# Optimization experiments

Hardware: AMD Instinct MI355X
Metric: run time of the kernel (lower is better)

## Reference

```python
import jax, jax.numpy as jnp
import numpy as np

PRECISION = 127.0  # number of discrete pulse-width levels per unit weight


def pwb_quantize(w):
    """PWBMapper: constrain weight to [-1, 1] and snap to `precision` levels."""
    return jnp.round(jnp.clip(w, -1.0, 1.0) * PRECISION) / PRECISION


def setup_inputs() -> dict:
    key = jax.random.key(0)
    kx, kw, kb = jax.random.split(key, 3)
    B, D_in, D_out = 32768, 1024, 128
    x = jax.random.normal(kx, (B, D_in), dtype=jnp.float32)
    # random_normal_initializer default stddev is small; scale a bit but keep in clip range
    W = jax.random.normal(kw, (D_in, D_out), dtype=jnp.float32) * 0.05
    b = jax.random.normal(kb, (D_out,), dtype=jnp.float32) * 0.05
    return {"x": x, "W": W, "b": b}


def reference(x, W, b):
    # Each neuron n.step(data) = dot(quantized weight column, data);
    # bias_neuron.step(e_i) = quantized bias[i].  Activation is identity (None).
    Wq = pwb_quantize(W)          # [D_in, D_out]
    bq = pwb_quantize(b)          # [D_out]
    return x @ Wq + bq            # [B, D_out]
```

## Files before the change

### kernel.cpp

```cpp
#include <hip/hip_runtime.h>
#include <cstdint>

#define K_DIM 1024
#define N_DIM 128
#define BM 64
#define BK 32
#define NT (K_DIM / BK)

typedef __attribute__((ext_vector_type(8))) short bf16x8;
typedef __attribute__((ext_vector_type(4))) float f32x4;
typedef unsigned short u16;
typedef unsigned int u32;

__device__ __forceinline__ float pwbq(float w) {
  w = fminf(fmaxf(w, -1.0f), 1.0f);
  return rintf(w * 127.0f) * (1.0f / 127.0f);
}

__device__ __forceinline__ u16 f2bf(float f) {
  union { float f; u32 u; } v; v.f = f;
  u32 r = v.u + 0x7FFFu + ((v.u >> 16) & 1u);
  return (u16)(r >> 16);
}

__global__ __launch_bounds__(256) void quantW_kernel(const float* __restrict__ W,
                                                     u16* __restrict__ Wimg) {
  int H = blockIdx.x * 256 + threadIdx.x;
  int t = H >> 12;
  int h = H & 4095;
  int col = h >> 5;
  int j = (h & 31) ^ ((col & 3) << 3);
  int k = t * BK + j;
  Wimg[H] = f2bf(pwbq(W[k * N_DIM + col]));
}

__global__ __launch_bounds__(256) void naive_kernel(const float* __restrict__ x,
                                                    const float* __restrict__ W,
                                                    const float* __restrict__ b,
                                                    float* __restrict__ out, int total) {
  int idx = blockIdx.x * 256 + threadIdx.x;
  if (idx >= total) return;
  int m = idx >> 7, n = idx & 127;
  float acc = pwbq(b[n]);
  for (int k = 0; k < K_DIM; ++k)
    acc = fmaf(x[(size_t)m * K_DIM + k], pwbq(W[k * N_DIM + n]), acc);
  out[idx] = acc;
}

__global__ __launch_bounds__(256, 2) void pwb_gemm(
    const float* __restrict__ x,
    const u16* __restrict__ Wimg,
    const float* __restrict__ bias,
    float* __restrict__ out) {

  __shared__ __align__(16) float As[4][BM * BK];
  __shared__ __align__(16) u16   Bs[4][N_DIM * BK];

  const int tid  = threadIdx.x;
  const int lane = tid & 63;
  const int wid  = tid >> 6;
  const int wm   = wid >> 1;
  const int wn   = wid & 1;
  const int m0   = blockIdx.x * BM;
  const int l15  = lane & 15;
  const int lg   = lane >> 4;

  auto stage = [&](int s, int t) {
#pragma unroll
    for (int i = 0; i < 2; ++i) {
      int cd  = i * 256 + tid;
      int row = cd >> 3;
      int cs  = (cd & 7) ^ (row & 7);
      const float* srcA = x + (size_t)(m0 + row) * K_DIM + t * BK + cs * 4;
      __builtin_amdgcn_global_load_lds(
          (const __attribute__((address_space(1))) void*)srcA,
          (__attribute__((address_space(3))) void*)(&As[s][cd * 4]), 16, 0, 0);
    }
#pragma unroll
    for (int i = 0; i < 2; ++i) {
      int cd = i * 256 + tid;
      const u16* srcB = Wimg + (size_t)t * (N_DIM * BK) + cd * 8;
      __builtin_amdgcn_global_load_lds(
          (const __attribute__((address_space(1))) void*)srcB,
          (__attribute__((address_space(3))) void*)(&Bs[s][cd * 8]), 16, 0, 0);
    }
  };

  f32x4 acc[2][4] = {};

  stage(0, 0);
  stage(1, 1);

#pragma unroll 2
  for (int t = 0; t < NT; ++t) {
    const int buf = t & 3;
    if (t + 2 < NT) {
      stage((t + 2) & 3, t + 2);
      asm volatile("s_waitcnt vmcnt(8)" ::: "memory");
    } else if (t + 1 < NT) {
      asm volatile("s_waitcnt vmcnt(4)" ::: "memory");
    } else {
      asm volatile("s_waitcnt vmcnt(0)" ::: "memory");
    }
    asm volatile("s_barrier" ::: "memory");

    bf16x8 a[2];
#pragma unroll
    for (int q = 0; q < 2; ++q) {
      int row  = wm * 32 + q * 16 + l15;
      int base = row * 128 + lg * 32;
      int sw   = (row & 7) << 4;
      f32x4 f0 = *(const f32x4*)((const char*)&As[buf][0] + (base ^ sw));
      f32x4 f1 = *(const f32x4*)((const char*)&As[buf][0] + ((base + 16) ^ sw));
      union { bf16x8 v; u16 h[8]; } pa;
#pragma unroll
      for (int j = 0; j < 4; ++j) {
        pa.h[j]     = f2bf(f0[j]);
        pa.h[4 + j] = f2bf(f1[j]);
      }
      a[q] = pa.v;
    }

    bf16x8 bfr[4];
#pragma unroll
    for (int f = 0; f < 4; ++f) {
      int col  = wn * 64 + f * 16 + l15;
      int hoff = col * 32 + ((lg * 8) ^ ((col & 3) << 3));
      bfr[f] = *(const bf16x8*)(&Bs[buf][hoff]);
    }

#pragma unroll
    for (int q = 0; q < 2; ++q)
#pragma unroll
      for (int f = 0; f < 4; ++f)
        acc[q][f] = __builtin_amdgcn_mfma_f32_16x16x32_bf16(a[q], bfr[f], acc[q][f], 0, 0, 0);
  }

  float bq[4];
#pragma unroll
  for (int f = 0; f < 4; ++f) bq[f] = pwbq(bias[wn * 64 + f * 16 + l15]);

#pragma unroll
  for (int q = 0; q < 2; ++q) {
    int gr0 = m0 + wm * 32 + q * 16 + lg * 4;
#pragma unroll
    for (int f = 0; f < 4; ++f) {
      int gc = wn * 64 + f * 16 + l15;
#pragma unroll
      for (int j = 0; j < 4; ++j) {
        out[(size_t)(gr0 + j) * N_DIM + gc] = acc[q][f][j] + bq[f];
      }
    }
  }
}

extern "C" void kernel_launch(void* const* d_in, const int* in_sizes, int n_in,
                              void* d_out, int out_size, void* d_ws, size_t ws_size,
                              hipStream_t stream) {
  const float* x = (const float*)d_in[0];
  const float* W = (const float*)d_in[1];
  const float* b = (const float*)d_in[2];
  float* out = (float*)d_out;

  const int M = in_sizes[0] / K_DIM;
  const int grid = M / BM;

  const size_t need = (size_t)K_DIM * N_DIM * sizeof(u16);
  if (d_ws != nullptr && ws_size >= need) {
    u16* Wimg = (u16*)d_ws;
    quantW_kernel<<<(K_DIM * N_DIM) / 256, 256, 0, stream>>>(W, Wimg);
    pwb_gemm<<<grid, 256, 0, stream>>>(x, Wimg, b, out);
  } else {
    int total = M * N_DIM;
    naive_kernel<<<(total + 255) / 256, 256, 0, stream>>>(x, W, b, out, total);
  }
}
```

Measured before the change: 35.70 us.

## Replace LDS-staged GEMM with direct global-to-register loads and smaller tiles

Removes shared memory staging and barriers: each wave loads its A rows and B fragments directly from global memory into registers with a three-slot register prefetch ring. The M tile shrinks to 32 rows so there are more blocks, with each of the four waves owning 32 output columns, and occupancy is raised to four blocks per CU. Conversion to bf16 now uses the packed HIP intrinsic. The trade-off is that the x rows are loaded redundantly by all four waves (four times the global/L2 traffic for A), with no barrier-based reuse through LDS.

```diff
diff --git a/kernel.cpp b/kernel.cpp
--- a/kernel.cpp
+++ b/kernel.cpp
@@ -1,11 +1,11 @@
 #include <hip/hip_runtime.h>
+#include <hip/hip_bf16.h>
 #include <cstdint>
 
 #define K_DIM 1024
 #define N_DIM 128
-#define BM 64
-#define BK 32
-#define NT (K_DIM / BK)
+#define BM 32
+#define NT 32
 
 typedef __attribute__((ext_vector_type(8))) short bf16x8;
 typedef __attribute__((ext_vector_type(4))) float f32x4;
@@ -27,11 +27,9 @@
                                                      u16* __restrict__ Wimg) {
   int H = blockIdx.x * 256 + threadIdx.x;
   int t = H >> 12;
-  int h = H & 4095;
-  int col = h >> 5;
-  int j = (h & 31) ^ ((col & 3) << 3);
-  int k = t * BK + j;
-  Wimg[H] = f2bf(pwbq(W[k * N_DIM + col]));
+  int col = (H >> 5) & 127;
+  int j = H & 31;
+  Wimg[H] = f2bf(pwbq(W[(t * 32 + j) * N_DIM + col]));
 }
 
 __global__ __launch_bounds__(256) void naive_kernel(const float* __restrict__ x,
@@ -47,105 +45,79 @@
   out[idx] = acc;
 }
 
-__global__ __launch_bounds__(256, 2) void pwb_gemm(
+__global__ __launch_bounds__(256, 4) void pwb_gemm(
     const float* __restrict__ x,
     const u16* __restrict__ Wimg,
     const float* __restrict__ bias,
     float* __restrict__ out) {
 
-  __shared__ __align__(16) float As[4][BM * BK];
-  __shared__ __align__(16) u16   Bs[4][N_DIM * BK];
-
   const int tid  = threadIdx.x;
   const int lane = tid & 63;
   const int wid  = tid >> 6;
-  const int wm   = wid >> 1;
-  const int wn   = wid & 1;
   const int m0   = blockIdx.x * BM;
   const int l15  = lane & 15;
   const int lg   = lane >> 4;
 
-  auto stage = [&](int s, int t) {
+  const float* pa0 = x + (size_t)(m0 + l15) * K_DIM + lg * 8;
+  const float* pa1 = pa0 + (size_t)16 * K_DIM;
+  const u16*   pb0 = Wimg + (wid * 32 + l15) * 32 + lg * 8;
+  const u16*   pb1 = pb0 + 16 * 32;
+
+  f32x4  af[3][2][2];
+  bf16x8 bf[3][2];
+  f32x4  acc[2][2] = {};
+
+#define LOADT(S, T)                                                        \
+  do {                                                                     \
+    const float* a0 = pa0 + (T) * 32;                                      \
+    const float* a1 = pa1 + (T) * 32;                                      \
+    af[S][0][0] = *(const f32x4*)(a0);                                     \
+    af[S][0][1] = *(const f32x4*)(a0 + 4);                                 \
+    af[S][1][0] = *(const f32x4*)(a1);                                     \
+    af[S][1][1] = *(const f32x4*)(a1 + 4);                                 \
+    bf[S][0] = *(const bf16x8*)(pb0 + (T) * 4096);                         \
+    bf[S][1] = *(const bf16x8*)(pb1 + (T) * 4096);                         \
+  } while (0)
+
+  LOADT(0, 0);
+  LOADT(1, 1);
+
 #pragma unroll
-    for (int i = 0; i < 2; ++i) {
-      int cd  = i * 256 + tid;
-      int row = cd >> 3;
-      int cs  = (cd & 7) ^ (row & 7);
-      const float* srcA = x + (size_t)(m0 + row) * K_DIM + t * BK + cs * 4;
-      __builtin_amdgcn_global_load_lds(
-          (const __attribute__((address_space(1))) void*)srcA,
-          (__attribute__((address_space(3))) void*)(&As[s][cd * 4]), 16, 0, 0);
-    }
-#pragma unroll
-    for (int i = 0; i < 2; ++i) {
-      int cd = i * 256 + tid;
-      const u16* srcB = Wimg + (size_t)t * (N_DIM * BK) + cd * 8;
-      __builtin_amdgcn_global_load_lds(
-          (const __attribute__((address_space(1))) void*)srcB,
-          (__attribute__((address_space(3))) void*)(&Bs[s][cd * 8]), 16, 0, 0);
-    }
-  };
-
-  f32x4 acc[2][4] = {};
-
-  stage(0, 0);
-  stage(1, 1);
-
-#pragma unroll 2
   for (int t = 0; t < NT; ++t) {
-    const int buf = t & 3;
-    if (t + 2 < NT) {
-      stage((t + 2) & 3, t + 2);
-      asm volatile("s_waitcnt vmcnt(8)" ::: "memory");
-    } else if (t + 1 < NT) {
-      asm volatile("s_waitcnt vmcnt(4)" ::: "memory");
-    } else {
-      asm volatile("s_waitcnt vmcnt(0)" ::: "memory");
-    }
-    asm volatile("s_barrier" ::: "memory");
+    const int s = t % 3;
+    if (t + 2 < NT) LOADT((t + 2) % 3, t + 2);
 
     bf16x8 a[2];
 #pragma unroll
     for (int q = 0; q < 2; ++q) {
-      int row  = wm * 32 + q * 16 + l15;
-      int base = row * 128 + lg * 32;
-      int sw   = (row & 7) << 4;
-      f32x4 f0 = *(const f32x4*)((const char*)&As[buf][0] + (base ^ sw));
-      f32x4 f1 = *(const f32x4*)((const char*)&As[buf][0] + ((base + 16) ^ sw));
-      union { bf16x8 v; u16 h[8]; } pa;
-#pragma unroll
-      for (int j = 0; j < 4; ++j) {
-        pa.h[j]     = f2bf(f0[j]);
-        pa.h[4 + j] = f2bf(f1[j]);
-      }
+      union { bf16x8 v; __hip_bfloat162 p[4]; } pa;
+      f32x4 f0 = af[s][q][0];
+      f32x4 f1 = af[s][q][1];
+      pa.p[0] = __float22bfloat162_rn(make_float2(f0[0], f0[1]));
+      pa.p[1] = __float22bfloat162_rn(make_float2(f0[2], f0[3]));
+      pa.p[2] = __float22bfloat162_rn(make_float2(f1[0], f1[1]));
+      pa.p[3] = __float22bfloat162_rn(make_float2(f1[2], f1[3]));
       a[q] = pa.v;
-    }
-
-    bf16x8 bfr[4];
-#pragma unroll
-    for (int f = 0; f < 4; ++f) {
-      int col  = wn * 64 + f * 16 + l15;
-      int hoff = col * 32 + ((lg * 8) ^ ((col & 3) << 3));
-      bfr[f] = *(const bf16x8*)(&Bs[buf][hoff]);
     }
 
 #pragma unroll
     for (int q = 0; q < 2; ++q)
 #pragma unroll
-      for (int f = 0; f < 4; ++f)
-        acc[q][f] = __builtin_amdgcn_mfma_f32_16x16x32_bf16(a[q], bfr[f], acc[q][f], 0, 0, 0);
+      for (int f = 0; f < 2; ++f)
+        acc[q][f] = __builtin_amdgcn_mfma_f32_16x16x32_bf16(a[q], bf[s][f], acc[q][f], 0, 0, 0);
   }
+#undef LOADT
 
-  float bq[4];
+  float bq[2];
 #pragma unroll
-  for (int f = 0; f < 4; ++f) bq[f] = pwbq(bias[wn * 64 + f * 16 + l15]);
+  for (int f = 0; f < 2; ++f) bq[f] = pwbq(bias[wid * 32 + f * 16 + l15]);
 
 #pragma unroll
   for (int q = 0; q < 2; ++q) {
-    int gr0 = m0 + wm * 32 + q * 16 + lg * 4;
+    int gr0 = m0 + q * 16 + lg * 4;
 #pragma unroll
-    for (int f = 0; f < 4; ++f) {
-      int gc = wn * 64 + f * 16 + l15;
+    for (int f = 0; f < 2; ++f) {
+      int gc = wid * 32 + f * 16 + l15;
 #pragma unroll
       for (int j = 0; j < 4; ++j) {
         out[(size_t)(gr0 + j) * N_DIM + gc] = acc[q][f][j] + bq[f];
```

Result: slower. 82.04 us (+129.8%).

## Halve M tile, use triple-buffered LDS with single barrier, packed bf16 conversion

Applied to the files above, without the earlier changes.

Reduces the block row tile from 64 to 32 rows, so each wave handles one 16-row A fragment, and raises the launch bound to 4 blocks per SIMD group. The LDS ring shrinks from four to three stages. The next-next stage is now issued after the barrier, which lets a single barrier per iteration protect buffer reuse. The manual fp32-to-bf16 rounding is replaced by packed __float22bfloat162_rn conversions, and the K loop is fully unrolled. The goal is more occupancy and more blocks to hide memory latency, at the cost of reloading the full W tile for every 32 rows, which doubles B traffic per output row.

```diff
diff --git a/kernel.cpp b/kernel.cpp
--- a/kernel.cpp
+++ b/kernel.cpp
@@ -1,9 +1,10 @@
 #include <hip/hip_runtime.h>
+#include <hip/hip_bf16.h>
 #include <cstdint>
 
 #define K_DIM 1024
 #define N_DIM 128
-#define BM 64
+#define BM 32
 #define BK 32
 #define NT (K_DIM / BK)
 
@@ -47,14 +48,14 @@
   out[idx] = acc;
 }
 
-__global__ __launch_bounds__(256, 2) void pwb_gemm(
+__global__ __launch_bounds__(256, 4) void pwb_gemm(
     const float* __restrict__ x,
     const u16* __restrict__ Wimg,
     const float* __restrict__ bias,
     float* __restrict__ out) {
 
-  __shared__ __align__(16) float As[4][BM * BK];
-  __shared__ __align__(16) u16   Bs[4][N_DIM * BK];
+  __shared__ __align__(16) float As[3][BM * BK];
+  __shared__ __align__(16) u16   Bs[3][N_DIM * BK];
 
   const int tid  = threadIdx.x;
   const int lane = tid & 63;
@@ -66,9 +67,8 @@
   const int lg   = lane >> 4;
 
   auto stage = [&](int s, int t) {
-#pragma unroll
-    for (int i = 0; i < 2; ++i) {
-      int cd  = i * 256 + tid;
+    {
+      int cd  = tid;
       int row = cd >> 3;
       int cs  = (cd & 7) ^ (row & 7);
       const float* srcA = x + (size_t)(m0 + row) * K_DIM + t * BK + cs * 4;
@@ -86,71 +86,50 @@
     }
   };
 
-  f32x4 acc[2][4] = {};
+  f32x4 acc[4] = {};
 
   stage(0, 0);
   stage(1, 1);
 
-#pragma unroll 2
+#pragma unroll
   for (int t = 0; t < NT; ++t) {
-    const int buf = t & 3;
-    if (t + 2 < NT) {
-      stage((t + 2) & 3, t + 2);
-      asm volatile("s_waitcnt vmcnt(8)" ::: "memory");
-    } else if (t + 1 < NT) {
-      asm volatile("s_waitcnt vmcnt(4)" ::: "memory");
-    } else {
-      asm volatile("s_waitcnt vmcnt(0)" ::: "memory");
-    }
+    const int buf = t % 3;
+
+    if (t + 1 < NT) asm volatile("s_waitcnt vmcnt(3)" ::: "memory");
+    else            asm volatile("s_waitcnt vmcnt(0)" ::: "memory");
     asm volatile("s_barrier" ::: "memory");
 
-    bf16x8 a[2];
-#pragma unroll
-    for (int q = 0; q < 2; ++q) {
-      int row  = wm * 32 + q * 16 + l15;
-      int base = row * 128 + lg * 32;
-      int sw   = (row & 7) << 4;
-      f32x4 f0 = *(const f32x4*)((const char*)&As[buf][0] + (base ^ sw));
-      f32x4 f1 = *(const f32x4*)((const char*)&As[buf][0] + ((base + 16) ^ sw));
-      union { bf16x8 v; u16 h[8]; } pa;
-#pragma unroll
-      for (int j = 0; j < 4; ++j) {
-        pa.h[j]     = f2bf(f0[j]);
-        pa.h[4 + j] = f2bf(f1[j]);
-      }
-      a[q] = pa.v;
-    }
+    if (t + 2 < NT) stage((t + 2) % 3, t + 2);
 
-    bf16x8 bfr[4];
+    const int row  = wm * 16 + l15;
+    const int base = row * 128 + lg * 32;
+    const int sw   = (row & 7) << 4;
+    f32x4 f0 = *(const f32x4*)((const char*)&As[buf][0] + (base ^ sw));
+    f32x4 f1 = *(const f32x4*)((const char*)&As[buf][0] + ((base + 16) ^ sw));
+    union { bf16x8 v; __hip_bfloat162 p[4]; } pa;
+    pa.p[0] = __float22bfloat162_rn(make_float2(f0[0], f0[1]));
+    pa.p[1] = __float22bfloat162_rn(make_float2(f0[2], f0[3]));
+    pa.p[2] = __float22bfloat162_rn(make_float2(f1[0], f1[1]));
+    pa.p[3] = __float22bfloat162_rn(make_float2(f1[2], f1[3]));
+    bf16x8 a = pa.v;
+
 #pragma unroll
     for (int f = 0; f < 4; ++f) {
       int col  = wn * 64 + f * 16 + l15;
       int hoff = col * 32 + ((lg * 8) ^ ((col & 3) << 3));
-      bfr[f] = *(const bf16x8*)(&Bs[buf][hoff]);
+      bf16x8 bfr = *(const bf16x8*)(&Bs[buf][hoff]);
+      acc[f] = __builtin_amdgcn_mfma_f32_16x16x32_bf16(a, bfr, acc[f], 0, 0, 0);
     }
+  }
 
 #pragma unroll
-    for (int q = 0; q < 2; ++q)
+  for (int f = 0; f < 4; ++f) {
+    const int gc = wn * 64 + f * 16 + l15;
+    const float bq = pwbq(bias[gc]);
+    const int gr0 = m0 + wm * 16 + lg * 4;
 #pragma unroll
-      for (int f = 0; f < 4; ++f)
-        acc[q][f] = __builtin_amdgcn_mfma_f32_16x16x32_bf16(a[q], bfr[f], acc[q][f], 0, 0, 0);
-  }
-
-  float bq[4];
-#pragma unroll
-  for (int f = 0; f < 4; ++f) bq[f] = pwbq(bias[wn * 64 + f * 16 + l15]);
-
-#pragma unroll
-  for (int q = 0; q < 2; ++q) {
-    int gr0 = m0 + wm * 32 + q * 16 + lg * 4;
-#pragma unroll
-    for (int f = 0; f < 4; ++f) {
-      int gc = wn * 64 + f * 16 + l15;
-#pragma unroll
-      for (int j = 0; j < 4; ++j) {
-        out[(size_t)(gr0 + j) * N_DIM + gc] = acc[q][f][j] + bq[f];
-      }
-    }
+    for (int j = 0; j < 4; ++j)
+      out[(size_t)(gr0 + j) * N_DIM + gc] = acc[f][j] + bq;
   }
 }
 
```

After: 34.90 us. -2.2%, faster.
